# Kernel optimization log

Measured on AMD Instinct MI355X. Metric: run time of the kernel, lower is better.

Reference implementation:

```python
import jax, jax.numpy as jnp
import numpy as np
from jax import lax

# Static configuration (torch module passes these as shape lists / init kwargs)
RATE = 2
FUSE_K = 3
SOFTMAX_SCALE = 10.0
B, L, C = 1, 4096, 64
HS = WS = 64            # downscaled foreground spatial (int_fs)
HB = WB = 64            # background patch grid (int_bs); HB*WB == L
KP = 2 * RATE           # raw patch kernel size = 4
PAD_T = 1               # torch conv_transpose2d padding


def setup_inputs() -> dict:
    key = jax.random.key(0)
    ks = jax.random.split(key, 6)
    raw_w = jax.random.normal(ks[0], (B, L, C, KP, KP), jnp.float32) * 0.1
    mm = (jax.random.uniform(ks[1], (B, L, 1, 1)) > 0.5).astype(jnp.float32)
    scores = jax.random.normal(ks[2], (B, L, HS, WS), jnp.float32)
    w1 = jax.random.normal(ks[3], (C, C, 3, 3), jnp.float32) * 0.05
    b1 = jnp.zeros((C,), jnp.float32)
    w2 = jax.random.normal(ks[4], (C, C, 3, 3), jnp.float32) * 0.05
    b2 = jnp.zeros((C,), jnp.float32)
    return {"raw_w": raw_w, "mm": mm, "scores": scores,
            "w1": w1, "b1": b1, "w2": w2, "b2": b2}


def _conv2d(x, w, b=None, padding=1):
    y = lax.conv_general_dilated(x, w, (1, 1), [(padding, padding)] * 2,
                                 dimension_numbers=('NCHW', 'OIHW', 'NCHW'))
    if b is not None:
        y = y + b[None, :, None, None]
    return y


def _fuse(yi):
    # Diagonal-kernel fusion (DeepFill): treat scores as a (HB*WB) x (HS*WS) image
    # and convolve with an identity (eye) kernel along both pairings.
    k = FUSE_K
    eye = jnp.eye(k, dtype=yi.dtype)[None, None]  # [1,1,k,k]
    x = yi.reshape(B, 1, HB * WB, HS * WS)
    x = _conv2d(x, eye, padding=k // 2)
    x = x.reshape(B, HB, WB, HS, WS).transpose(0, 2, 1, 4, 3)
    x = x.reshape(B, 1, WB * HB, WS * HS)
    x = _conv2d(x, eye, padding=k // 2)
    x = x.reshape(B, WB, HB, WS, HS).transpose(0, 2, 1, 4, 3)  # [B,HB,WB,HS,WS]
    return x.reshape(B, L, HS, WS)


def _deconv_item(y_b, w_b):
    # torch F.conv_transpose2d(y, w, stride=RATE, padding=PAD_T) for one item.
    # y_b: [L,HS,WS], w_b: [L,C,KP,KP] -> [C, RATE*HS, RATE*WS]
    wt = jnp.flip(w_b, axis=(-2, -1)).transpose(1, 0, 2, 3)  # [C,L,KP,KP]
    pad = KP - 1 - PAD_T
    out = lax.conv_general_dilated(y_b[None], wt, (1, 1), [(pad, pad)] * 2,
                                   lhs_dilation=(RATE, RATE),
                                   dimension_numbers=('NCHW', 'OIHW', 'NCHW'))
    return out[0] / 4.0  # overlap normalization (4 = number of overlapping patches)


def reference(raw_w, mm, scores, w1, b1, w2, b2):
    yi = _fuse(scores)
    yi = jax.nn.softmax(yi * mm * SOFTMAX_SCALE, axis=1) * mm  # softmax over L patches
    y = jax.vmap(_deconv_item)(yi, raw_w)  # [B, C, RATE*HS, RATE*WS]
    # trailing Conv+ELU x2 (self.out)
    y = jax.nn.elu(_conv2d(y, w1, b1))
    y = jax.nn.elu(_conv2d(y, w2, b2))
    return y
```

## Files before the change

kernel.cpp:

```cpp
#include <hip/hip_runtime.h>
#include <hip/hip_bf16.h>
#include <math.h>

#define NL 4096
#define NQ 4096
#define SCALE 10.0f

typedef __bf16 bf16x8 __attribute__((ext_vector_type(8)));
typedef float  f32x4  __attribute__((ext_vector_type(4)));
typedef float  f32x4u __attribute__((ext_vector_type(4), aligned(4)));

#define GLOAD_LDS16(gp, lp)                                                        \
    __builtin_amdgcn_global_load_lds((const __attribute__((address_space(1))) void*)(gp), \
                                     (__attribute__((address_space(3))) void*)(lp), \
                                     16, 0, 0)

__device__ __forceinline__ void ldtap(const float* __restrict__ S, int r, int c0,
                                      float t[4]) {
    if (r < 0 || r >= 4096) { t[0] = t[1] = t[2] = t[3] = 0.f; return; }
    const float* p = S + (size_t)r * 4096;
    if (c0 >= 0 && c0 <= 4092) {
        f32x4u v = *(const f32x4u*)(p + c0);
        t[0] = v.x; t[1] = v.y; t[2] = v.z; t[3] = v.w;
    } else {
        #pragma unroll
        for (int i = 0; i < 4; ++i) {
            int c = c0 + i;
            t[i] = (c >= 0 && c < 4096) ? p[c] : 0.f;
        }
    }
}

__global__ __launch_bounds__(256) void fuseD(const float* __restrict__ S,
                                             float* __restrict__ F) {
    int lin = blockIdx.x;
    int l = (lin & 7) * 512 + (lin >> 3);
    int hb = l >> 6, wb = l & 63;
    int rowb[3]; bool rok[3];
    #pragma unroll
    for (int d = 0; d < 3; ++d) {
        int h2 = hb + d - 1;
        if (h2 >= 0 && h2 <= 63) { rowb[d] = h2 * 64 + wb; rok[d] = true; }
        else if (h2 < 0)         { rowb[d] = 4031 + wb;    rok[d] = (wb >= 1); }
        else                     { rowb[d] = 1 + wb;       rok[d] = (wb <= 62); }
    }
    float* Fr = F + (size_t)l * 4096;

    #pragma unroll
    for (int cc = 0; cc < 4; ++cc) {
        int q0 = (cc * 256 + threadIdx.x) * 4;
        int hs = q0 >> 6, ws0 = q0 & 63;
        float acc[4] = {0.f, 0.f, 0.f, 0.f};
        #pragma unroll
        for (int d = 0; d < 3; ++d) {
            if (!rok[d]) continue;
            int s2 = hs + d - 1;
            int colb; float m0 = 1.f, m3 = 1.f;
            if (s2 >= 0 && s2 <= 63) colb = s2 * 64 + ws0;
            else if (s2 < 0) { colb = 4031 + ws0; if (ws0 == 0)  m0 = 0.f; }
            else             { colb = 1 + ws0;    if (ws0 == 60) m3 = 0.f; }
            float s3[4] = {0.f, 0.f, 0.f, 0.f};
            #pragma unroll
            for (int d1 = -1; d1 <= 1; ++d1) {
                float t[4];
                ldtap(S, rowb[d] + d1, colb + d1, t);
                s3[0] += t[0]; s3[1] += t[1]; s3[2] += t[2]; s3[3] += t[3];
            }
            acc[0] += m0 * s3[0]; acc[1] += s3[1]; acc[2] += s3[2]; acc[3] += m3 * s3[3];
        }
        *(float4*)&Fr[q0] = make_float4(acc[0], acc[1], acc[2], acc[3]);
    }
}

__global__ __launch_bounds__(256) void softPart(const float* __restrict__ F,
                                                const float* __restrict__ mm,
                                                float* __restrict__ Pm,
                                                float* __restrict__ Ps) {
    int qt = blockIdx.x, lc = blockIdx.y;
    int qo = threadIdx.x & 63, lg = threadIdx.x >> 6;
    int q = qt * 64 + qo;
    __shared__ float red[4][64];

    float sv[32];
    float m = -1e30f;
    #pragma unroll
    for (int i = 0; i < 32; ++i) {
        int l = lc * 128 + i * 4 + lg;
        float s = F[(size_t)l * 4096 + q] * mm[l] * SCALE;
        sv[i] = s;
        m = fmaxf(m, s);
    }
    red[lg][qo] = m;
    __syncthreads();
    m = fmaxf(fmaxf(red[0][qo], red[1][qo]), fmaxf(red[2][qo], red[3][qo]));
    __syncthreads();

    float sum = 0.f;
    #pragma unroll
    for (int i = 0; i < 32; ++i) sum += __expf(sv[i] - m);
    red[lg][qo] = sum;
    __syncthreads();
    if (lg == 0) {
        sum = red[0][qo] + red[1][qo] + red[2][qo] + red[3][qo];
        Pm[lc * 4096 + q] = m;
        Ps[lc * 4096 + q] = sum;
    }
}

__global__ void softComb(const float* __restrict__ Pm, const float* __restrict__ Ps,
                         float* __restrict__ Qm, float* __restrict__ Qi) {
    int q = blockIdx.x * 256 + threadIdx.x;
    float M = -1e30f;
    #pragma unroll
    for (int i = 0; i < 32; ++i) M = fmaxf(M, Pm[i * 4096 + q]);
    float S = 0.f;
    #pragma unroll
    for (int i = 0; i < 32; ++i) S += Ps[i * 4096 + q] * __expf(Pm[i * 4096 + q] - M);
    Qm[q] = M;
    Qi[q] = 1.0f / S;
}

__global__ __launch_bounds__(256) void normTransP(const float* __restrict__ F,
                                                  const float* __restrict__ mm,
                                                  const float* __restrict__ Qm,
                                                  const float* __restrict__ Qi,
                                                  __hip_bfloat16* __restrict__ Pt) {
    __shared__ float T[64][65];
    int qt = blockIdx.x, lt = blockIdx.y;
    int c = threadIdx.x & 63;
    int q = qt * 64 + c;
    float qm = Qm[q], qi = Qi[q];
    #pragma unroll
    for (int p = 0; p < 16; ++p) {
        int r = p * 4 + (threadIdx.x >> 6);
        int l = lt * 64 + r;
        float mml = mm[l];
        float s = F[(size_t)l * 4096 + q] * mml * SCALE - qm;
        T[r][c] = mml * __expf(s) * qi;
    }
    __syncthreads();
    #pragma unroll
    for (int p = 0; p < 16; ++p) {
        int r = p * 4 + (threadIdx.x >> 6);
        Pt[(size_t)(qt * 64 + r) * 4096 + lt * 64 + c] = (__hip_bfloat16)T[c][r];
    }
}

__global__ __launch_bounds__(256) void transW(const float* __restrict__ Wsrc,
                                              __hip_bfloat16* __restrict__ Wt) {
    __shared__ float T[64][65];
    int nt = blockIdx.x, kt = blockIdx.y;
    int c = threadIdx.x & 63;
    #pragma unroll
    for (int p = 0; p < 16; ++p) {
        int r = p * 4 + (threadIdx.x >> 6);
        T[r][c] = Wsrc[(size_t)(kt * 64 + r) * 1024 + nt * 64 + c];
    }
    __syncthreads();
    #pragma unroll
    for (int p = 0; p < 16; ++p) {
        int r = p * 4 + (threadIdx.x >> 6);
        int n_new = (r & 15) * 64 + nt * 4 + (r >> 4);
        Wt[(size_t)n_new * 4096 + kt * 64 + c] = (__hip_bfloat16)T[c][r];
    }
}

__global__ void transWc(const float* __restrict__ Wsrc, __hip_bfloat16* __restrict__ Wd) {
    int t = blockIdx.x * 256 + threadIdx.x;
    int kyx = t >> 12;
    int co = (t >> 6) & 63;
    int ci = t & 63;
    Wd[t] = (__hip_bfloat16)Wsrc[co * 576 + ci * 9 + kyx];
}

__global__ __launch_bounds__(256) void gemmMfmaK(const __hip_bfloat16* __restrict__ Ab,
                                                 const __hip_bfloat16* __restrict__ Bb,
                                                 float* __restrict__ C0,
                                                 float* __restrict__ C1) {
    __shared__ __align__(16) __hip_bfloat16 As[2][128][32];
    __shared__ __align__(16) __hip_bfloat16 Bs[2][128][32];
    int lin = blockIdx.x;
    int wid = (lin & 7) * 64 + (lin >> 3);
    int bm = wid & 31;
    int bn = (wid >> 5) & 7;
    int bz = wid >> 8;
    int bm0 = bm * 128, bn0 = bn * 128;
    size_t kbase = (size_t)bz * 2048;
    float* Cm = bz ? C1 : C0;

    int tid = threadIdx.x;
    int lane = tid & 63, w = tid >> 6;
    int wm = (w >> 1) * 64, wn = (w & 1) * 64;

    int srow = w * 32 + (lane >> 2);
    int scol = (((lane & 3) ^ ((lane >> 3) & 3))) * 8;
    const __hip_bfloat16* ga0 = Ab + (size_t)(bm0 + srow) * 4096 + kbase + scol;
    const __hip_bfloat16* ga1 = Ab + (size_t)(bm0 + srow + 16) * 4096 + kbase + scol;
    const __hip_bfloat16* gb0 = Bb + (size_t)(bn0 + srow) * 4096 + kbase + scol;
    const __hip_bfloat16* gb1 = Bb + (size_t)(bn0 + srow + 16) * 4096 + kbase + scol;

    f32x4 acc[4][4] = {};
    int fm = lane & 15;
    int fkz = (((lane >> 4) ^ ((lane >> 1) & 3))) * 8;

    GLOAD_LDS16(ga0, &As[0][w * 32][0]);
    GLOAD_LDS16(ga1, &As[0][w * 32 + 16][0]);
    GLOAD_LDS16(gb0, &Bs[0][w * 32][0]);
    GLOAD_LDS16(gb1, &Bs[0][w * 32 + 16][0]);
    __syncthreads();

    int buf = 0;
    for (int t = 0; t < 64; ++t) {
        if (t + 1 < 64) {
            int k0 = (t + 1) * 32;
            GLOAD_LDS16(ga0 + k0, &As[buf ^ 1][w * 32][0]);
            GLOAD_LDS16(ga1 + k0, &As[buf ^ 1][w * 32 + 16][0]);
            GLOAD_LDS16(gb0 + k0, &Bs[buf ^ 1][w * 32][0]);
            GLOAD_LDS16(gb1 + k0, &Bs[buf ^ 1][w * 32 + 16][0]);
        }
        bf16x8 af[4], bfr[4];
        #pragma unroll
        for (int i = 0; i < 4; ++i)
            af[i] = *(const bf16x8*)&As[buf][wm + i * 16 + fm][fkz];
        #pragma unroll
        for (int j = 0; j < 4; ++j)
            bfr[j] = *(const bf16x8*)&Bs[buf][wn + j * 16 + fm][fkz];
        #pragma unroll
        for (int i = 0; i < 4; ++i)
            #pragma unroll
            for (int j = 0; j < 4; ++j)
                acc[i][j] = __builtin_amdgcn_mfma_f32_16x16x32_bf16(af[i], bfr[j], acc[i][j], 0, 0, 0);
        __syncthreads();
        buf ^= 1;
    }

    #pragma unroll
    for (int i = 0; i < 4; ++i) {
        #pragma unroll
        for (int j = 0; j < 4; ++j) {
            int row = bm0 + wm + i * 16 + (lane >> 4) * 4;
            int col = bn0 + wn + j * 16 + (lane & 15);
            #pragma unroll
            for (int r = 0; r < 4; ++r)
                Cm[(size_t)(row + r) * 1024 + col] = acc[i][j][r];
        }
    }
}

__global__ void scatterD(const float* __restrict__ Mo, const float* __restrict__ Mo2,
                         __hip_bfloat16* __restrict__ Xp) {
    int c = threadIdx.x & 63;
    int pix = blockIdx.x * 4 + (threadIdx.x >> 6);
    int ox = pix & 127, oy = pix >> 7;
    float acc = 0.f;
    #pragma unroll
    for (int ky = 0; ky < 4; ++ky) {
        int ty = oy + 1 - ky;
        if (ty & 1) continue;
        int iy = ty >> 1;
        if (iy < 0 || iy >= 64) continue;
        #pragma unroll
        for (int kx = 0; kx < 4; ++kx) {
            int txx = ox + 1 - kx;
            if (txx & 1) continue;
            int ix = txx >> 1;
            if (ix < 0 || ix >= 64) continue;
            size_t off = (size_t)(iy * 64 + ix) * 1024 + (ky * 4 + kx) * 64 + c;
            acc += Mo[off] + Mo2[off];
        }
    }
    Xp[((size_t)(oy + 1) * 130 + ox + 1) * 64 + c] = (__hip_bfloat16)(acc * 0.25f);
}

template <int MODE>
__global__ __launch_bounds__(256) void convMfma(const __hip_bfloat16* __restrict__ Xp,
                                                const __hip_bfloat16* __restrict__ Wc,
                                                const float* __restrict__ Bi,
                                                __hip_bfloat16* __restrict__ Yp,
                                                float* __restrict__ Yo) {
    int tid = threadIdx.x, lane = tid & 63, w = tid >> 6;
    int y = blockIdx.x >> 1, x0 = (blockIdx.x & 1) * 64;
    int co0 = w * 16;
    int fl = lane & 15, fh = lane >> 4;

    bf16x8 wb[3][3][2];
    #pragma unroll
    for (int ky = 0; ky < 3; ++ky)
        #pragma unroll
        for (int kx = 0; kx < 3; ++kx)
            #pragma unroll
            for (int kc = 0; kc < 2; ++kc)
                wb[ky][kx][kc] = *(const bf16x8*)&Wc[(size_t)((ky * 3 + kx) * 64 + co0 + fl) * 64 + kc * 32 + fh * 8];

    f32x4 acc[4] = {};
    #pragma unroll
    for (int ky = 0; ky < 3; ++ky) {
        #pragma unroll
        for (int kx = 0; kx < 3; ++kx) {
            const __hip_bfloat16* xrow = Xp + ((size_t)(y + ky) * 130 + x0 + kx) * 64;
            #pragma unroll
            for (int kc = 0; kc < 2; ++kc) {
                #pragma unroll
                for (int mt = 0; mt < 4; ++mt) {
                    bf16x8 af = *(const bf16x8*)&xrow[(mt * 16 + fl) * 64 + kc * 32 + fh * 8];
                    acc[mt] = __builtin_amdgcn_mfma_f32_16x16x32_bf16(af, wb[ky][kx][kc], acc[mt], 0, 0, 0);
                }
            }
        }
    }

    float bias = Bi[co0 + fl];
    #pragma unroll
    for (int mt = 0; mt < 4; ++mt) {
        int xb = x0 + mt * 16 + fh * 4;
        if (MODE == 0) {
            #pragma unroll
            for (int r = 0; r < 4; ++r) {
                float v = acc[mt][r] + bias;
                v = v > 0.f ? v : expm1f(v);
                Yp[((size_t)(y + 1) * 130 + xb + r + 1) * 64 + co0 + fl] = (__hip_bfloat16)v;
            }
        } else {
            float4 o;
            float* op = (float*)&o;
            #pragma unroll
            for (int r = 0; r < 4; ++r) {
                float v = acc[mt][r] + bias;
                op[r] = v > 0.f ? v : expm1f(v);
            }
            *(float4*)&Yo[(size_t)(co0 + fl) * 16384 + y * 128 + xb] = o;
        }
    }
}

extern "C" void kernel_launch(void* const* d_in, const int* in_sizes, int n_in,
                              void* d_out, int out_size, void* d_ws, size_t ws_size,
                              hipStream_t stream) {
    const float* raw_w  = (const float*)d_in[0];
    const float* mm     = (const float*)d_in[1];
    const float* scores = (const float*)d_in[2];
    const float* w1     = (const float*)d_in[3];
    const float* b1     = (const float*)d_in[4];
    const float* w2     = (const float*)d_in[5];
    const float* b2     = (const float*)d_in[6];
    float* out = (float*)d_out;

    char* ws = (char*)d_ws;
    __hip_bfloat16* Pt  = (__hip_bfloat16*)ws;
    __hip_bfloat16* Wt  = (__hip_bfloat16*)(ws + (32ull << 20));
    float*          Pm  = (float*)(ws + (40ull << 20));
    float*          Ps  = (float*)(ws + (40ull << 20) + (512u << 10));
    float*          Qm  = (float*)(ws + (41ull << 20));
    float*          Qi  = (float*)(ws + (41ull << 20) + (64u << 10));
    __hip_bfloat16* Wc1 = (__hip_bfloat16*)(ws + (41ull << 20) + (256u << 10));
    __hip_bfloat16* Wc2 = (__hip_bfloat16*)(ws + (41ull << 20) + (384u << 10));
    float*          Mo  = (float*)(ws + (42ull << 20));
    __hip_bfloat16* Xp  = (__hip_bfloat16*)(ws + (58ull << 20));
    __hip_bfloat16* Y1p = (__hip_bfloat16*)(ws + (61ull << 20));
    float*          F   = (float*)(ws + (64ull << 20));
    float*          Mo2 = (float*)(ws + (64ull << 20));

    const size_t XP_BYTES = 130ull * 130 * 64 * sizeof(__hip_bfloat16);

    fuseD<<<4096, 256, 0, stream>>>(scores, F);
    transW<<<dim3(16, 64), 256, 0, stream>>>(raw_w, Wt);
    transWc<<<144, 256, 0, stream>>>(w1, Wc1);
    transWc<<<144, 256, 0, stream>>>(w2, Wc2);
    softPart<<<dim3(64, 32), 256, 0, stream>>>(F, mm, Pm, Ps);
    softComb<<<16, 256, 0, stream>>>(Pm, Ps, Qm, Qi);
    normTransP<<<dim3(64, 64), 256, 0, stream>>>(F, mm, Qm, Qi, Pt);
    gemmMfmaK<<<512, 256, 0, stream>>>(Pt, Wt, Mo, Mo2);
    hipMemsetAsync(Xp, 0, XP_BYTES, stream);
    hipMemsetAsync(Y1p, 0, XP_BYTES, stream);
    scatterD<<<4096, 256, 0, stream>>>(Mo, Mo2, Xp);
    convMfma<0><<<256, 256, 0, stream>>>(Xp, Wc1, b1, Y1p, nullptr);
    convMfma<1><<<256, 256, 0, stream>>>(Y1p, Wc2, b2, nullptr, out);
}
```

Measured before the change: 177.0 us.

## Compute four patch rows per block in fuseD with register and shuffle reuse

The diagonal-fusion kernel now has each block produce four consecutive L rows instead of one. It loads a 6-row window of aligned float4s once and builds the shifted horizontal taps with wavefront shuffles, instead of issuing nine unaligned loads per output. The goal is to cut redundant global and L2 traffic in the first stage. The cost is higher register pressure, more complicated edge and wraparound handling, and a quarter as many blocks.

```diff
diff --git a/kernel.cpp b/kernel.cpp
--- a/kernel.cpp
+++ b/kernel.cpp
@@ -15,60 +15,116 @@
                                      (__attribute__((address_space(3))) void*)(lp), \
                                      16, 0, 0)
 
-__device__ __forceinline__ void ldtap(const float* __restrict__ S, int r, int c0,
-                                      float t[4]) {
-    if (r < 0 || r >= 4096) { t[0] = t[1] = t[2] = t[3] = 0.f; return; }
-    const float* p = S + (size_t)r * 4096;
-    if (c0 >= 0 && c0 <= 4092) {
-        f32x4u v = *(const f32x4u*)(p + c0);
-        t[0] = v.x; t[1] = v.y; t[2] = v.z; t[3] = v.w;
-    } else {
-        #pragma unroll
-        for (int i = 0; i < 4; ++i) {
-            int c = c0 + i;
-            t[i] = (c >= 0 && c < 4096) ? p[c] : 0.f;
-        }
-    }
-}
-
 __global__ __launch_bounds__(256) void fuseD(const float* __restrict__ S,
                                              float* __restrict__ F) {
     int lin = blockIdx.x;
-    int l = (lin & 7) * 512 + (lin >> 3);
-    int hb = l >> 6, wb = l & 63;
-    int rowb[3]; bool rok[3];
+    int blk = (lin & 7) * 128 + (lin >> 3);
+    int l0 = blk * 4;
+    int hb = l0 >> 6, wb0 = l0 & 63;
+    int tid = threadIdx.x, lane = tid & 63;
+
+    int rowbase[3]; float wm[3][4];
     #pragma unroll
     for (int d = 0; d < 3; ++d) {
         int h2 = hb + d - 1;
-        if (h2 >= 0 && h2 <= 63) { rowb[d] = h2 * 64 + wb; rok[d] = true; }
-        else if (h2 < 0)         { rowb[d] = 4031 + wb;    rok[d] = (wb >= 1); }
-        else                     { rowb[d] = 1 + wb;       rok[d] = (wb <= 62); }
-    }
-    float* Fr = F + (size_t)l * 4096;
-
-    #pragma unroll
+        #pragma unroll
+        for (int i = 0; i < 4; ++i) wm[d][i] = 1.f;
+        if (h2 >= 0 && h2 <= 63) rowbase[d] = h2 * 64 + wb0;
+        else if (h2 < 0) {
+            rowbase[d] = 4031 + wb0;
+            #pragma unroll
+            for (int i = 0; i < 4; ++i) wm[d][i] = (wb0 + i >= 1) ? 1.f : 0.f;
+        } else {
+            rowbase[d] = 1 + wb0;
+            #pragma unroll
+            for (int i = 0; i < 4; ++i) wm[d][i] = (wb0 + i <= 62) ? 1.f : 0.f;
+        }
+    }
+
     for (int cc = 0; cc < 4; ++cc) {
-        int q0 = (cc * 256 + threadIdx.x) * 4;
+        int q0 = (cc * 256 + tid) * 4;
         int hs = q0 >> 6, ws0 = q0 & 63;
-        float acc[4] = {0.f, 0.f, 0.f, 0.f};
+        f32x4 z4 = {0.f, 0.f, 0.f, 0.f};
+        f32x4 acc0 = z4, acc1 = z4, acc2 = z4, acc3 = z4;
+
         #pragma unroll
         for (int d = 0; d < 3; ++d) {
-            if (!rok[d]) continue;
             int s2 = hs + d - 1;
-            int colb; float m0 = 1.f, m3 = 1.f;
-            if (s2 >= 0 && s2 <= 63) colb = s2 * 64 + ws0;
-            else if (s2 < 0) { colb = 4031 + ws0; if (ws0 == 0)  m0 = 0.f; }
-            else             { colb = 1 + ws0;    if (ws0 == 60) m3 = 0.f; }
-            float s3[4] = {0.f, 0.f, 0.f, 0.f};
-            #pragma unroll
-            for (int d1 = -1; d1 <= 1; ++d1) {
-                float t[4];
-                ldtap(S, rowb[d] + d1, colb + d1, t);
-                s3[0] += t[0]; s3[1] += t[1]; s3[2] += t[2]; s3[3] += t[3];
-            }
-            acc[0] += m0 * s3[0]; acc[1] += s3[1]; acc[2] += s3[2]; acc[3] += m3 * s3[3];
-        }
-        *(float4*)&Fr[q0] = make_float4(acc[0], acc[1], acc[2], acc[3]);
+            bool cw = (s2 < 0) || (s2 > 63);
+            int colb = cw ? ((s2 < 0 ? 4031 : 1) + ws0) : (q0 + (d - 1) * 64);
+            int cb = cw ? colb - 1 : colb;
+
+            f32x4 v[6], v2[6];
+            #pragma unroll
+            for (int r = 0; r < 6; ++r) {
+                int rr = rowbase[d] - 1 + r;
+                v[r] = z4;
+                if (rr >= 0 && rr < 4096)
+                    v[r] = *(const f32x4u*)(S + (size_t)rr * 4096 + cb);
+            }
+            if (cw) {
+                #pragma unroll
+                for (int r = 0; r < 6; ++r) {
+                    int rr = rowbase[d] - 1 + r;
+                    v2[r] = z4;
+                    if (rr >= 0 && rr < 4096)
+                        v2[r] = *(const f32x4u*)(S + (size_t)rr * 4096 + colb + 1);
+                }
+            }
+
+            float lm[4], rm[4];
+            #pragma unroll
+            for (int r = 0; r < 4; ++r) lm[r] = __shfl_up(v[r][3], 1);
+            #pragma unroll
+            for (int r = 0; r < 4; ++r) rm[r] = __shfl_down(v[r + 2][0], 1);
+            if (!cw) {
+                if (lane == 0 || colb == 0) {
+                    #pragma unroll
+                    for (int r = 0; r < 4; ++r) {
+                        int rr = rowbase[d] - 1 + r;
+                        lm[r] = (colb > 0 && rr >= 0 && rr < 4096)
+                                ? S[(size_t)rr * 4096 + colb - 1] : 0.f;
+                    }
+                }
+                if (lane == 63 || colb + 4 >= 4096) {
+                    #pragma unroll
+                    for (int r = 0; r < 4; ++r) {
+                        int rr = rowbase[d] + 1 + r;
+                        rm[r] = (colb + 4 < 4096 && rr >= 0 && rr < 4096)
+                                ? S[(size_t)rr * 4096 + colb + 4] : 0.f;
+                    }
+                }
+            }
+
+            f32x4 t[4];
+            if (!cw) {
+                #pragma unroll
+                for (int i = 0; i < 4; ++i) {
+                    f32x4 Lv = { lm[i], v[i][0], v[i][1], v[i][2] };
+                    f32x4 Cv = v[i + 1];
+                    f32x4 Rv = { v[i + 2][1], v[i + 2][2], v[i + 2][3], rm[i] };
+                    t[i] = Lv + Cv + Rv;
+                }
+            } else {
+                #pragma unroll
+                for (int i = 0; i < 4; ++i) {
+                    f32x4 Lv = v[i];
+                    f32x4 Cv = { v[i+1][1], v[i+1][2], v[i+1][3], v2[i+1][2] };
+                    f32x4 Rv = v2[i + 2];
+                    t[i] = Lv + Cv + Rv;
+                }
+                if (s2 < 0 && ws0 == 0) { t[0][0] = 0.f; t[1][0] = 0.f; t[2][0] = 0.f; t[3][0] = 0.f; }
+                if (s2 > 63 && ws0 == 60) { t[0][3] = 0.f; t[1][3] = 0.f; t[2][3] = 0.f; t[3][3] = 0.f; }
+            }
+            acc0 += wm[d][0] * t[0];
+            acc1 += wm[d][1] * t[1];
+            acc2 += wm[d][2] * t[2];
+            acc3 += wm[d][3] * t[3];
+        }
+        *(f32x4*)(F + (size_t)(l0 + 0) * 4096 + q0) = acc0;
+        *(f32x4*)(F + (size_t)(l0 + 1) * 4096 + q0) = acc1;
+        *(f32x4*)(F + (size_t)(l0 + 2) * 4096 + q0) = acc2;
+        *(f32x4*)(F + (size_t)(l0 + 3) * 4096 + q0) = acc3;
     }
 }
 
@@ -362,7 +418,7 @@
 
     const size_t XP_BYTES = 130ull * 130 * 64 * sizeof(__hip_bfloat16);
 
-    fuseD<<<4096, 256, 0, stream>>>(scores, F);
+    fuseD<<<1024, 256, 0, stream>>>(scores, F);
     transW<<<dim3(16, 64), 256, 0, stream>>>(raw_w, Wt);
     transWc<<<144, 256, 0, stream>>>(w1, Wc1);
     transWc<<<144, 256, 0, stream>>>(w2, Wc2);
```

Result: no change. 177.4 us (+0.2%).
